# Kernel tuning notes

Measured on AMD Instinct MI355X. Metric: run time of the kernel, lower is better.

The kernel has to match this reference:

```python
import jax, jax.numpy as jnp
import numpy as np

B, NR, NF, NH, NFH, D, HID = 32, 32, 128, 64, 64, 32, 256


def setup_inputs() -> dict:
    key = jax.random.key(0)
    ks = jax.random.split(key, 16)

    def w(k, o, i):
        return (jax.random.normal(k, (o, i), jnp.float32) / np.sqrt(i)).astype(jnp.float32)

    inp = {
        "robot": jax.random.normal(ks[0], (B, NR, D), jnp.float32),
        "frontier": jax.random.normal(ks[1], (B, NF, D), jnp.float32),
        "robot_history": jax.random.normal(ks[2], (B, NH, D), jnp.float32),
        "frontier_history": jax.random.normal(ks[3], (B, NFH, D), jnp.float32),
        "robot_frontier": jax.random.uniform(ks[4], (B, NR, NF), jnp.float32),
        "robot_past": jax.random.uniform(ks[5], (B, NR, NH), jnp.float32),
        "frontier_past": jax.random.uniform(ks[6], (B, NF, NFH), jnp.float32),
        # parameters (torch Linear convention: weight [out, in])
        "Wq": w(ks[7], D, D), "bq": jnp.zeros(D, jnp.float32),
        "Wk": w(ks[8], D, D), "bk": jnp.zeros(D, jnp.float32),
        "Wv": w(ks[9], D, D), "bv": jnp.zeros(D, jnp.float32),
        "Wn1": w(ks[10], HID, 2 * D), "bn1": jnp.zeros(HID, jnp.float32),
        "Wn2": w(ks[11], D, HID), "bn2": jnp.zeros(D, jnp.float32),
        "We1": w(ks[12], HID, 2 * D + 1), "be1": jnp.zeros(HID, jnp.float32),
        "We2": w(ks[13], 1, HID), "be2": jnp.zeros(1, jnp.float32),
    }
    return inp


def reference(robot, frontier, robot_history, frontier_history, robot_frontier,
              robot_past, frontier_past, Wq, bq, Wk, bk, Wv, bv,
              Wn1, bn1, Wn2, bn2, We1, be1, We2, be2):
    def lin(x, W, b):
        return x @ W.T + b

    def nmlp(h):
        return lin(jax.nn.relu(lin(h, Wn1, bn1)), Wn2, bn2)

    def emlp(h):
        return lin(jax.nn.relu(lin(h, We1, be1)), We2, be2)

    def intra(x):  # x: [b, n, D]
        q, k, v = lin(x, Wq, bq), lin(x, Wk, bk), lin(x, Wv, bv)
        e = jax.nn.softmax(jnp.einsum('bnd,bmd->bnm', q, k), axis=-1)
        agg = jnp.einsum('bnm,bmd->bnd', e, v)
        return x + nmlp(jnp.concatenate([x, agg], axis=-1))

    def inter(x, y, dis):  # x: [b,Nx,D], y: [b,Ny,D], dis: [b,Nx,Ny]
        xq, yk, yv = lin(x, Wq, bq), lin(y, Wk, bk), lin(y, Wv, bv)
        b, Nx, _ = x.shape
        Ny = y.shape[1]
        r_i = jnp.broadcast_to(xq[:, :, None, :], (b, Nx, Ny, D))
        f_j = jnp.broadcast_to(yk[:, None, :, :], (b, Nx, Ny, D))
        edge_input = jnp.concatenate([r_i, f_j, dis[..., None]], axis=-1)  # [b,Nx,Ny,65]
        score = emlp(edge_input)[..., 0]                                   # [b,Nx,Ny]
        e = jax.nn.softmax(score, axis=-1)
        agg = jnp.einsum('bnm,bmd->bnd', e, yv)
        x = x + nmlp(jnp.concatenate([x, agg], axis=-1))
        return e, x

    robot = intra(robot)
    frontier = intra(frontier)           # == per-sample intra on [1,Nf,D]
    robot_history = intra(robot_history)
    frontier_history = intra(frontier_history)
    _, robot = inter(robot, robot_history, robot_past)
    _, new_frontier = inter(frontier, frontier_history, frontier_past)
    edge, robot = inter(robot, new_frontier, robot_frontier)
    # original returns the intra-transformed frontier (split_frontier), not new_frontier
    return (robot, frontier, robot_history, frontier_history, edge)
```

## Files before the change

### kernel.cpp

```cpp
#include <hip/hip_runtime.h>

#define BATCH 32
#define NRr 32
#define NFf 128
#define NHh 64
#define NFHh 64
#define TI 4

__device__ __forceinline__ float dot4(float4 a, float4 b) {
    return fmaf(a.x, b.x, fmaf(a.y, b.y, fmaf(a.z, b.z, a.w * b.w)));
}

__global__ __launch_bounds__(256) void intra_kernel(
    const float* __restrict__ robot, const float* __restrict__ frontier,
    const float* __restrict__ rhist, const float* __restrict__ fhist,
    const float* __restrict__ Wq, const float* __restrict__ bq,
    const float* __restrict__ Wk, const float* __restrict__ bk,
    const float* __restrict__ Wv, const float* __restrict__ bv,
    const float* __restrict__ Wn1, const float* __restrict__ bn1,
    const float* __restrict__ Wn2, const float* __restrict__ bn2,
    float* __restrict__ o_robot, float* __restrict__ o_frontier,
    float* __restrict__ o_rh, float* __restrict__ o_fh)
{
    __shared__ __align__(16) float sXc[1024];
    __shared__ __align__(16) float sQ[1024];
    __shared__ __align__(16) float sAgg[1024];
    __shared__ __align__(16) float sS[4224];
    __shared__ __align__(16) float sKT[4128];
    __shared__ __align__(16) float sVT[8192];

    const int blk = blockIdx.x, tid = threadIdx.x;
    const float* xin; float* xout; int N, lgN, b, chunk;
    if (blk < 32)       { xin=robot;    xout=o_robot;    N=32;  lgN=5; b=blk;          chunk=0; }
    else if (blk < 160) { xin=frontier; xout=o_frontier; N=128; lgN=7; b=(blk-32)>>2;  chunk=(blk-32)&3; }
    else if (blk < 224) { xin=rhist;    xout=o_rh;       N=64;  lgN=6; b=(blk-160)>>1; chunk=(blk-160)&1; }
    else                { xin=fhist;    xout=o_fh;       N=64;  lgN=6; b=(blk-224)>>1; chunk=(blk-224)&1; }

    const int P = N + 4;
    const float* xb = xin + (size_t)b * N * 32;
    const int r0 = chunk << 5;
    const int d = tid & 31;

    {
        int idx = tid;
        #pragma unroll
        for (int it = 0; it < 4; ++it, idx += 256)
            sXc[idx] = xb[(r0 << 5) + idx];
    }

    {
        const float4* wk4 = (const float4*)(Wk + (d << 5));
        const float4* wv4 = (const float4*)(Wv + (d << 5));
        float4 wk[8], wv[8];
        #pragma unroll
        for (int k = 0; k < 8; ++k) { wk[k] = wk4[k]; wv[k] = wv4[k]; }
        const float bkd = bk[d], bvd = bv[d];
        for (int idx = tid; idx < (N << 5); idx += 256) {
            int j = idx >> 5;
            const float4* xr = (const float4*)(xb + (j << 5));
            float aK = bkd, aV = bvd;
            #pragma unroll
            for (int k = 0; k < 8; ++k) {
                float4 xv = xr[k];
                aK += dot4(wk[k], xv);
                aV += dot4(wv[k], xv);
            }
            sKT[d * 129 + j] = aK;
            sVT[(j << 5) + d] = aV;
        }
    }
    __syncthreads();

    {
        const float4* wq4 = (const float4*)(Wq + (d << 5));
        float4 wq[8];
        #pragma unroll
        for (int k = 0; k < 8; ++k) wq[k] = wq4[k];
        const float bqd = bq[d];
        int idx = tid;
        #pragma unroll
        for (int it = 0; it < 4; ++it, idx += 256) {
            int r = idx >> 5;
            const float4* xr = (const float4*)(sXc + (r << 5));
            float a = bqd;
            #pragma unroll
            for (int k = 0; k < 8; ++k) a += dot4(wq[k], xr[k]);
            sQ[idx] = a;
        }
    }
    __syncthreads();

    for (int idx = tid; idx < (N << 5); idx += 256) {
        int r = idx >> lgN, j = idx & (N - 1);
        const float* qr = sQ + (r << 5);
        float a = 0.f;
        #pragma unroll
        for (int e = 0; e < 32; ++e) a = fmaf(qr[e], sKT[e * 129 + j], a);
        sS[r * P + j] = a;
    }
    __syncthreads();

    {
        int r = tid >> 3, l = tid & 7;
        float* row = sS + r * P;
        float m = -1e30f;
        for (int j = l; j < N; j += 8) m = fmaxf(m, row[j]);
        m = fmaxf(m, __shfl_xor(m, 4));
        m = fmaxf(m, __shfl_xor(m, 2));
        m = fmaxf(m, __shfl_xor(m, 1));
        float s = 0.f;
        for (int j = l; j < N; j += 8) { float ev = __expf(row[j] - m); row[j] = ev; s += ev; }
        s += __shfl_xor(s, 4); s += __shfl_xor(s, 2); s += __shfl_xor(s, 1);
        float inv = 1.0f / s;
        for (int j = l; j < N; j += 8) row[j] *= inv;
    }
    __syncthreads();

    {
        int idx = tid;
        #pragma unroll
        for (int it = 0; it < 4; ++it, idx += 256) {
            int r = idx >> 5;
            const float* er = sS + r * P;
            float a = 0.f;
            for (int j = 0; j < N; ++j) a = fmaf(er[j], sVT[(j << 5) + d], a);
            sAgg[idx] = a;
        }
    }
    __syncthreads();

    float* sT = sVT;
    {
        const float4* w14 = (const float4*)(Wn1 + (tid << 6));
        float4 w1r[16];
        #pragma unroll
        for (int k = 0; k < 16; ++k) w1r[k] = w14[k];
        const float b1 = bn1[tid];
        for (int r = 0; r < 32; ++r) {
            const float4* xr = (const float4*)(sXc + (r << 5));
            const float4* ar = (const float4*)(sAgg + (r << 5));
            float a = b1;
            #pragma unroll
            for (int k = 0; k < 8; ++k) a += dot4(w1r[k], xr[k]);
            #pragma unroll
            for (int k = 0; k < 8; ++k) a += dot4(w1r[8 + k], ar[k]);
            sT[(r << 8) + tid] = fmaxf(a, 0.f);
        }
    }
    __syncthreads();

    {
        const int rg = tid >> 5;
        float acc[4] = {0.f, 0.f, 0.f, 0.f};
        #pragma unroll
        for (int hc = 0; hc < 4; ++hc) {
            const float4* w24 = (const float4*)(Wn2 + (d << 8) + (hc << 6));
            float4 w2r[16];
            #pragma unroll
            for (int k = 0; k < 16; ++k) w2r[k] = w24[k];
            #pragma unroll
            for (int p = 0; p < 4; ++p) {
                int r = rg + (p << 3);
                const float4* tr = (const float4*)(sT + (r << 8) + (hc << 6));
                float a = 0.f;
                #pragma unroll
                for (int k = 0; k < 16; ++k) a += dot4(w2r[k], tr[k]);
                acc[p] += a;
            }
        }
        const float b2 = bn2[d];
        #pragma unroll
        for (int p = 0; p < 4; ++p) {
            int r = rg + (p << 3);
            xout[((size_t)b * N << 5) + ((r0 + r) << 5) + d] = sXc[(r << 5) + d] + b2 + acc[p];
        }
    }
}

__global__ __launch_bounds__(256) void pre_y_kernel(
    const float* __restrict__ yA, int NyA, float* __restrict__ wOutA, float* __restrict__ yvOutA, int nBlkA,
    const float* __restrict__ yB, int NyB, float* __restrict__ wOutB, float* __restrict__ yvOutB,
    const float* __restrict__ Wk, const float* __restrict__ bk,
    const float* __restrict__ Wv, const float* __restrict__ bv,
    const float* __restrict__ We1)
{
    __shared__ __align__(16) float sY[256], sK[256];
    const int blk = blockIdx.x, tid = threadIdx.x;
    const float* y; int Ny; float* wOut; float* yvOut; int idx;
    if (blk < nBlkA) { y=yA; Ny=NyA; wOut=wOutA; yvOut=yvOutA; idx=blk; }
    else             { y=yB; Ny=NyB; wOut=wOutB; yvOut=yvOutB; idx=blk-nBlkA; }
    const int chunks = Ny >> 3;
    const int b = idx / chunks, j0 = (idx - b * chunks) << 3;

    sY[tid] = y[((size_t)(b * Ny + j0)) * 32 + tid];
    __syncthreads();

    {
        int jl = tid >> 5, dd = tid & 31;
        const float4* wk4 = (const float4*)(Wk + (dd << 5));
        const float4* wv4 = (const float4*)(Wv + (dd << 5));
        const float4* yr = (const float4*)(sY + (jl << 5));
        float aK = bk[dd], aV = bv[dd];
        #pragma unroll
        for (int k = 0; k < 8; ++k) {
            float4 yv4 = yr[k];
            aK += dot4(wk4[k], yv4);
            aV += dot4(wv4[k], yv4);
        }
        sK[(jl << 5) + dd] = aK;
        yvOut[((size_t)(b * Ny + j0 + jl)) * 32 + dd] = aV;
    }
    __syncthreads();

    {
        const float* w1 = We1 + tid * 65 + 32;
        float acc[8] = {0,0,0,0,0,0,0,0};
        #pragma unroll
        for (int e = 0; e < 32; ++e) {
            float we = w1[e];
            #pragma unroll
            for (int jl = 0; jl < 8; ++jl)
                acc[jl] = fmaf(we, sK[(jl << 5) + e], acc[jl]);
        }
        float* wbase = wOut + (((size_t)b * 64 + (tid >> 2)) * Ny + j0) * 4 + (tid & 3);
        #pragma unroll
        for (int jl = 0; jl < 8; ++jl)
            wbase[jl << 2] = acc[jl];
    }
}

__global__ __launch_bounds__(256) void inter_main_kernel(
    const float* __restrict__ xA, int NxA, const float* __restrict__ wA, const float* __restrict__ yvA,
    int NyA, const float* __restrict__ disA, float* __restrict__ outA, float* __restrict__ eA,
    float* __restrict__ wPreA, float* __restrict__ yvPreA, int nBlkA,
    const float* __restrict__ xB, int NxB, const float* __restrict__ wB, const float* __restrict__ yvB,
    int NyB, const float* __restrict__ disB, float* __restrict__ outB, float* __restrict__ eB,
    float* __restrict__ wPreB, float* __restrict__ yvPreB,
    const float* __restrict__ Wq, const float* __restrict__ bq,
    const float* __restrict__ Wk, const float* __restrict__ bk,
    const float* __restrict__ Wv, const float* __restrict__ bv,
    const float* __restrict__ We1, const float* __restrict__ be1,
    const float* __restrict__ We2,
    const float* __restrict__ Wn1, const float* __restrict__ bn1,
    const float* __restrict__ Wn2, const float* __restrict__ bn2)
{
    __shared__ __align__(16) float sX[128];
    __shared__ __align__(16) float sQ[128];
    __shared__ __align__(16) float sAgg[128];
    __shared__ __align__(16) float sDis[512];
    __shared__ __align__(16) float sC[256];
    __shared__ __align__(16) float sW2[256];
    __shared__ __align__(16) float sS[512];
    __shared__ __align__(16) float sUT[1024];
    __shared__ __align__(16) float sPR[2048];
    __shared__ __align__(16) float sYV[4096];

    const int blk = blockIdx.x, tid = threadIdx.x;
    const float* x; int Nx; const float* w; const float* yv; int Ny;
    const float* dis; float* outp; float* ep; float* wPre; float* yvPre; int idx;
    if (blk < nBlkA) { x=xA; Nx=NxA; w=wA; yv=yvA; Ny=NyA; dis=disA; outp=outA; ep=eA; wPre=wPreA; yvPre=yvPreA; idx=blk; }
    else             { x=xB; Nx=NxB; w=wB; yv=yvB; Ny=NyB; dis=disB; outp=outB; ep=eB; wPre=wPreB; yvPre=yvPreB; idx=blk-nBlkA; }
    const int lgNy = (Ny == 128) ? 7 : 6;
    const int tiles = Nx >> 2;
    const int b = idx / tiles, i0 = (idx - b * tiles) << 2;
    const float* xrow = x + ((size_t)(b * Nx + i0)) * 32;

    if (tid < 128) sX[tid] = xrow[tid];
    if (tid < Ny) {
        int il = tid >> (lgNy - 2), jq = tid & ((Ny >> 2) - 1);
        ((float4*)sDis)[(il << 5) + jq] =
            ((const float4*)(dis + ((size_t)(b * Nx + i0 + il)) * Ny))[jq];
    }
    {
        const float4* yv4 = (const float4*)(yv + ((size_t)(b * Ny) << 5));
        for (int k = tid; k < (Ny << 3); k += 256)
            ((float4*)sYV)[k] = yv4[k];
    }
    __syncthreads();

    if (tid < 128) {
        int il = tid >> 5, dd = tid & 31;
        const float4* wq4 = (const float4*)(Wq + (dd << 5));
        const float4* xr = (const float4*)(sX + (il << 5));
        float a = bq[dd];
        #pragma unroll
        for (int k = 0; k < 8; ++k) a += dot4(wq4[k], xr[k]);
        sQ[tid] = a;
    }
    __syncthreads();

    {
        const float* w1 = We1 + tid * 65;
        const float b1 = be1[tid];
        float acc[TI];
        #pragma unroll
        for (int il = 0; il < TI; ++il) acc[il] = b1;
        #pragma unroll
        for (int e = 0; e < 32; ++e) {
            float we = w1[e];
            #pragma unroll
            for (int il = 0; il < TI; ++il)
                acc[il] = fmaf(we, sQ[(il << 5) + e], acc[il]);
        }
        #pragma unroll
        for (int il = 0; il < TI; ++il) sUT[(il << 8) + tid] = acc[il];
        sC[tid] = w1[64];
        sW2[tid] = We2[tid];
    }
    __syncthreads();

    const int wv = tid >> 6, lane = tid & 63;
    {
        const int hc0 = wv << 4;
        const float4* wT4 = (const float4*)w + (size_t)(b * 64) * Ny;
        const float4* c4p = (const float4*)sC;
        const float4* p4p = (const float4*)sW2;
        if (Ny == 64) {
            float dv[TI];
            #pragma unroll
            for (int il = 0; il < TI; ++il) dv[il] = sDis[(il << 7) + lane];
            float acc[TI] = {0.f, 0.f, 0.f, 0.f};
            #pragma unroll
            for (int t = 0; t < 16; ++t) {
                int hc = hc0 + t;
                float4 w4 = wT4[((size_t)hc << 6) + lane];
                float4 c4 = c4p[hc], p4 = p4p[hc];
                #pragma unroll
                for (int il = 0; il < TI; ++il) {
                    float4 u4 = ((const float4*)(sUT + (il << 8)))[hc];
                    acc[il] = fmaf(p4.x, fmaxf(fmaf(c4.x, dv[il], u4.x + w4.x), 0.f), acc[il]);
                    acc[il] = fmaf(p4.y, fmaxf(fmaf(c4.y, dv[il], u4.y + w4.y), 0.f), acc[il]);
                    acc[il] = fmaf(p4.z, fmaxf(fmaf(c4.z, dv[il], u4.z + w4.z), 0.f), acc[il]);
                    acc[il] = fmaf(p4.w, fmaxf(fmaf(c4.w, dv[il], u4.w + w4.w), 0.f), acc[il]);
                }
            }
            #pragma unroll
            for (int il = 0; il < TI; ++il)
                sPR[(wv << 9) + (il << 7) + lane] = acc[il];
        } else {
            float dv0[TI], dv1[TI];
            #pragma unroll
            for (int il = 0; il < TI; ++il) {
                dv0[il] = sDis[(il << 7) + lane];
                dv1[il] = sDis[(il << 7) + 64 + lane];
            }
            float acc0[TI] = {0.f, 0.f, 0.f, 0.f};
            float acc1[TI] = {0.f, 0.f, 0.f, 0.f};
            #pragma unroll
            for (int t = 0; t < 16; ++t) {
                int hc = hc0 + t;
                float4 wa = wT4[((size_t)hc << 7) + lane];
                float4 wb = wT4[((size_t)hc << 7) + 64 + lane];
                float4 c4 = c4p[hc], p4 = p4p[hc];
                #pragma unroll
                for (int il = 0; il < TI; ++il) {
                    float4 u4 = ((const float4*)(sUT + (il << 8)))[hc];
                    acc0[il] = fmaf(p4.x, fmaxf(fmaf(c4.x, dv0[il], u4.x + wa.x), 0.f), acc0[il]);
                    acc0[il] = fmaf(p4.y, fmaxf(fmaf(c4.y, dv0[il], u4.y + wa.y), 0.f), acc0[il]);
                    acc0[il] = fmaf(p4.z, fmaxf(fmaf(c4.z, dv0[il], u4.z + wa.z), 0.f), acc0[il]);
                    acc0[il] = fmaf(p4.w, fmaxf(fmaf(c4.w, dv0[il], u4.w + wa.w), 0.f), acc0[il]);
                    acc1[il] = fmaf(p4.x, fmaxf(fmaf(c4.x, dv1[il], u4.x + wb.x), 0.f), acc1[il]);
                    acc1[il] = fmaf(p4.y, fmaxf(fmaf(c4.y, dv1[il], u4.y + wb.y), 0.f), acc1[il]);
                    acc1[il] = fmaf(p4.z, fmaxf(fmaf(c4.z, dv1[il], u4.z + wb.z), 0.f), acc1[il]);
                    acc1[il] = fmaf(p4.w, fmaxf(fmaf(c4.w, dv1[il], u4.w + wb.w), 0.f), acc1[il]);
                }
            }
            #pragma unroll
            for (int il = 0; il < TI; ++il) {
                sPR[(wv << 9) + (il << 7) + lane] = acc0[il];
                sPR[(wv << 9) + (il << 7) + 64 + lane] = acc1[il];
            }
        }
    }
    __syncthreads();

    for (int k = tid; k < (TI << lgNy); k += 256) {
        int il = k >> lgNy, j = k & (Ny - 1);
        int o = (il << 7) + j;
        sS[o] = sPR[o] + sPR[512 + o] + sPR[1024 + o] + sPR[1536 + o];
    }
    __syncthreads();

    {
        float v0 = sS[(wv << 7) + lane];
        float v1 = (Ny == 128) ? sS[(wv << 7) + 64 + lane] : -1e30f;
        float m = fmaxf(v0, v1);
        #pragma unroll
        for (int msk = 32; msk; msk >>= 1) m = fmaxf(m, __shfl_xor(m, msk));
        float e0 = __expf(v0 - m);
        float e1 = (Ny == 128) ? __expf(v1 - m) : 0.f;
        float s = e0 + e1;
        #pragma unroll
        for (int msk = 32; msk; msk >>= 1) s += __shfl_xor(s, msk);
        float inv = 1.0f / s;
        e0 *= inv; e1 *= inv;
        sS[(wv << 7) + lane] = e0;
        if (Ny == 128) sS[(wv << 7) + 64 + lane] = e1;
        if (ep) {
            float* erow = ep + ((size_t)(b * Nx + i0 + wv)) * Ny;
            erow[lane] = e0;
            if (Ny == 128) erow[64 + lane] = e1;
        }
    }

    {
        const int dd = lane & 31, jg = lane >> 5;
        float p = 0.f;
        for (int j = jg; j < Ny; j += 2)
            p = fmaf(sS[(wv << 7) + j], sYV[(j << 5) + dd], p);
        p += __shfl_xor(p, 32);
        if (jg == 0) sAgg[(wv << 5) + dd] = p;
    }
    __syncthreads();

    {
        const float4* w14 = (const float4*)(Wn1 + (tid << 6));
        const float b1 = bn1[tid];
        float acc[TI];
        #pragma unroll
        for (int il = 0; il < TI; ++il) acc[il] = b1;
        #pragma unroll
        for (int k = 0; k < 8; ++k) {
            float4 wa = w14[k];
            #pragma unroll
            for (int il = 0; il < TI; ++il)
                acc[il] += dot4(wa, ((const float4*)(sX + (il << 5)))[k]);
        }
        #pragma unroll
        for (int k = 0; k < 8; ++k) {
            float4 wb = w14[8 + k];
            #pragma unroll
            for (int il = 0; il < TI; ++il)
                acc[il] += dot4(wb, ((const float4*)(sAgg + (il << 5)))[k]);
        }
        __syncthreads();
        #pragma unroll
        for (int il = 0; il < TI; ++il) sUT[(il << 8) + tid] = fmaxf(acc[il], 0.f);
    }
    __syncthreads();

    {
        const int hg = tid >> 5, dd = tid & 31;
        const float4* w24 = (const float4*)(Wn2 + (dd << 8) + (hg << 5));
        float4 w2r[8];
        #pragma unroll
        for (int k = 0; k < 8; ++k) w2r[k] = w24[k];
        float p[TI] = {0.f, 0.f, 0.f, 0.f};
        #pragma unroll
        for (int k = 0; k < 8; ++k) {
            #pragma unroll
            for (int il = 0; il < TI; ++il)
                p[il] += dot4(w2r[k], ((const float4*)(sUT + (il << 8) + (hg << 5)))[k]);
        }
        #pragma unroll
        for (int il = 0; il < TI; ++il) sPR[(hg << 7) + (il << 5) + dd] = p[il];
    }
    __syncthreads();
    if (tid < 128) {
        int il = tid >> 5, dd = tid & 31;
        float a = bn2[dd] + sX[tid];
        #pragma unroll
        for (int hg = 0; hg < 8; ++hg) a += sPR[(hg << 7) + tid];
        outp[((size_t)(b * Nx + i0 + il)) * 32 + dd] = a;
        if (wPre) sQ[tid] = a;
    }

    if (wPre) {
        __syncthreads();
        {
            int t = tid & 127, il = t >> 5, dd = t & 31;
            const float4* wm4 = (const float4*)(((tid < 128) ? Wk : Wv) + (dd << 5));
            const float4* orow = (const float4*)(sQ + (il << 5));
            float a = (tid < 128) ? bk[dd] : bv[dd];
            #pragma unroll
            for (int k = 0; k < 8; ++k) a += dot4(wm4[k], orow[k]);
            if (tid < 128) sS[il * 33 + dd] = a;
            else yvPre[(((size_t)(b * Nx + i0 + il)) << 5) + dd] = a;
        }
        __syncthreads();
        {
            const float* w1 = We1 + tid * 65 + 32;
            float acc[4] = {0.f, 0.f, 0.f, 0.f};
            #pragma unroll
            for (int e = 0; e < 32; ++e) {
                float we = w1[e];
                #pragma unroll
                for (int il = 0; il < 4; ++il)
                    acc[il] = fmaf(we, sS[il * 33 + e], acc[il]);
            }
            float* wbase = wPre + (((size_t)b * 64 + (tid >> 2)) * Nx + i0) * 4 + (tid & 3);
            #pragma unroll
            for (int il = 0; il < 4; ++il)
                wbase[il << 2] = acc[il];
        }
    }
}

extern "C" void kernel_launch(void* const* d_in, const int* in_sizes, int n_in,
                              void* d_out, int out_size, void* d_ws, size_t ws_size,
                              hipStream_t stream) {
    const float* robot          = (const float*)d_in[0];
    const float* frontier       = (const float*)d_in[1];
    const float* rh             = (const float*)d_in[2];
    const float* fh             = (const float*)d_in[3];
    const float* robot_frontier = (const float*)d_in[4];
    const float* robot_past     = (const float*)d_in[5];
    const float* frontier_past  = (const float*)d_in[6];
    const float* Wq  = (const float*)d_in[7];  const float* bq  = (const float*)d_in[8];
    const float* Wk  = (const float*)d_in[9];  const float* bk  = (const float*)d_in[10];
    const float* Wv  = (const float*)d_in[11]; const float* bv  = (const float*)d_in[12];
    const float* Wn1 = (const float*)d_in[13]; const float* bn1 = (const float*)d_in[14];
    const float* Wn2 = (const float*)d_in[15]; const float* bn2 = (const float*)d_in[16];
    const float* We1 = (const float*)d_in[17]; const float* be1 = (const float*)d_in[18];
    const float* We2 = (const float*)d_in[19];

    float* out = (float*)d_out;
    float* out_robot    = out;
    float* out_frontier = out + 32768;
    float* out_rh       = out + 163840;
    float* out_fh       = out + 229376;
    float* out_edge     = out + 294912;

    float* W = (float*)d_ws;
    float* robot1 = W;
    float* robot2 = W + 32768;
    float* nf     = W + 65536;
    float* w5     = W + 196608;
    float* yv5    = W + 720896;
    float* w6     = W + 786432;
    float* yv6    = W + 1310720;
    float* w7     = W + 1376256;
    float* yv7    = W + 2424832;

    intra_kernel<<<288, 256, 0, stream>>>(robot, frontier, rh, fh,
        Wq, bq, Wk, bk, Wv, bv, Wn1, bn1, Wn2, bn2,
        robot1, out_frontier, out_rh, out_fh);

    pre_y_kernel<<<512, 256, 0, stream>>>(
        out_rh, NHh, w5, yv5, BATCH * NHh / 8,
        out_fh, NFHh, w6, yv6,
        Wk, bk, Wv, bv, We1);

    inter_main_kernel<<<1280, 256, 0, stream>>>(
        robot1, NRr, w5, yv5, NHh, robot_past, robot2,
        (float*)nullptr, (float*)nullptr, (float*)nullptr, BATCH * (NRr / TI),
        out_frontier, NFf, w6, yv6, NFHh, frontier_past, nf,
        (float*)nullptr, w7, yv7,
        Wq, bq, Wk, bk, Wv, bv, We1, be1, We2, Wn1, bn1, Wn2, bn2);

    inter_main_kernel<<<256, 256, 0, stream>>>(
        robot2, NRr, w7, yv7, NFf, robot_frontier, out_robot, out_edge,
        (float*)nullptr, (float*)nullptr, BATCH * (NRr / TI),
        robot2, NRr, w7, yv7, NFf, robot_frontier, out_robot, out_edge,
        (float*)nullptr, (float*)nullptr,
        Wq, bq, Wk, bk, Wv, bv, We1, be1, We2, Wn1, bn1, Wn2, bn2);
}
```

Before: 210.0 us.

## Reassociate intra attention to skip K and V projections of all nodes

In the intra-attention kernel, K and V are no longer projected for every node. Scores are computed as (Q·Wk)·Xᵀ, which drops the bk term; that term is constant per row and cancels in the softmax. Aggregation is done as (softmax·X)·Wvᵀ + bv, which is valid because the softmax rows sum to one. This removes the per-block N×32 K/V projections, which were redundant across chunks, and replaces them with 32-row projections plus a transposed X copy in shared memory, which also shrinks the LDS footprint. The cost is extra small GEMM passes and barriers, and floating-point rounding that differs slightly from before.

```diff
diff --git a/kernel.cpp b/kernel.cpp
--- a/kernel.cpp
+++ b/kernel.cpp
@@ -24,10 +24,12 @@
 {
     __shared__ __align__(16) float sXc[1024];
     __shared__ __align__(16) float sQ[1024];
+    __shared__ __align__(16) float sQK[1024];
     __shared__ __align__(16) float sAgg[1024];
-    __shared__ __align__(16) float sS[4224];
-    __shared__ __align__(16) float sKT[4128];
-    __shared__ __align__(16) float sVT[8192];
+    __shared__ __align__(16) float sBig[8448];
+    float* sS  = sBig;
+    float* sXT = sBig + 4224;
+    float* sT  = sBig;
 
     const int blk = blockIdx.x, tid = threadIdx.x;
     const float* xin; float* xout; int N, lgN, b, chunk;
@@ -36,7 +38,7 @@
     else if (blk < 224) { xin=rhist;    xout=o_rh;       N=64;  lgN=6; b=(blk-160)>>1; chunk=(blk-160)&1; }
     else                { xin=fhist;    xout=o_fh;       N=64;  lgN=6; b=(blk-224)>>1; chunk=(blk-224)&1; }
 
-    const int P = N + 4;
+    const int P = N + 4, P2 = N + 1;
     const float* xb = xin + (size_t)b * N * 32;
     const int r0 = chunk << 5;
     const int d = tid & 31;
@@ -47,27 +49,9 @@
         for (int it = 0; it < 4; ++it, idx += 256)
             sXc[idx] = xb[(r0 << 5) + idx];
     }
-
-    {
-        const float4* wk4 = (const float4*)(Wk + (d << 5));
-        const float4* wv4 = (const float4*)(Wv + (d << 5));
-        float4 wk[8], wv[8];
-        #pragma unroll
-        for (int k = 0; k < 8; ++k) { wk[k] = wk4[k]; wv[k] = wv4[k]; }
-        const float bkd = bk[d], bvd = bv[d];
-        for (int idx = tid; idx < (N << 5); idx += 256) {
-            int j = idx >> 5;
-            const float4* xr = (const float4*)(xb + (j << 5));
-            float aK = bkd, aV = bvd;
-            #pragma unroll
-            for (int k = 0; k < 8; ++k) {
-                float4 xv = xr[k];
-                aK += dot4(wk[k], xv);
-                aV += dot4(wv[k], xv);
-            }
-            sKT[d * 129 + j] = aK;
-            sVT[(j << 5) + d] = aV;
-        }
+    for (int idx = tid; idx < (N << 5); idx += 256) {
+        int j = idx >> 5, d2 = idx & 31;
+        sXT[d2 * P2 + j] = xb[idx];
     }
     __syncthreads();
 
@@ -90,12 +74,27 @@
     }
     __syncthreads();
 
+    {
+        int idx = tid;
+        #pragma unroll
+        for (int it = 0; it < 4; ++it, idx += 256) {
+            int r = idx >> 5, e = idx & 31;
+            const float* qr = sQ + (r << 5);
+            float a = 0.f;
+            #pragma unroll
+            for (int dd2 = 0; dd2 < 32; ++dd2)
+                a = fmaf(Wk[dd2 * 32 + e], qr[dd2], a);
+            sQK[idx] = a;
+        }
+    }
+    __syncthreads();
+
     for (int idx = tid; idx < (N << 5); idx += 256) {
         int r = idx >> lgN, j = idx & (N - 1);
-        const float* qr = sQ + (r << 5);
+        const float* qr = sQK + (r << 5);
         float a = 0.f;
         #pragma unroll
-        for (int e = 0; e < 32; ++e) a = fmaf(qr[e], sKT[e * 129 + j], a);
+        for (int e = 0; e < 32; ++e) a = fmaf(qr[e], sXT[e * P2 + j], a);
         sS[r * P + j] = a;
     }
     __syncthreads();
@@ -120,16 +119,35 @@
         int idx = tid;
         #pragma unroll
         for (int it = 0; it < 4; ++it, idx += 256) {
+            int r = idx >> 5, d2 = idx & 31;
+            const float* er = sS + r * P;
+            const float* xtr = sXT + d2 * P2;
+            float a = 0.f;
+            for (int j = 0; j < N; ++j) a = fmaf(er[j], xtr[j], a);
+            sQ[idx] = a;
+        }
+    }
+    __syncthreads();
+
+    {
+        const float4* wv4 = (const float4*)(Wv + (d << 5));
+        float4 wv[8];
+        #pragma unroll
+        for (int k = 0; k < 8; ++k) wv[k] = wv4[k];
+        const float bvd = bv[d];
+        int idx = tid;
+        #pragma unroll
+        for (int it = 0; it < 4; ++it, idx += 256) {
             int r = idx >> 5;
-            const float* er = sS + r * P;
-            float a = 0.f;
-            for (int j = 0; j < N; ++j) a = fmaf(er[j], sVT[(j << 5) + d], a);
+            const float4* zr = (const float4*)(sQ + (r << 5));
+            float a = bvd;
+            #pragma unroll
+            for (int k = 0; k < 8; ++k) a += dot4(wv[k], zr[k]);
             sAgg[idx] = a;
         }
     }
     __syncthreads();
 
-    float* sT = sVT;
     {
         const float4* w14 = (const float4*)(Wn1 + (tid << 6));
         float4 w1r[16];
```

Measured after the change: 204.0 us. -2.9%, faster.
